# Performance work log

Hardware: AMD Instinct MI355X
Metric: run time of the kernel (lower is better)

Reference implementation:

```python
import jax, jax.numpy as jnp
import numpy as np

B, L, D = 2, 1024, 768
NH, HD = 12, 64
NL = 6
MLP = 3072
THETA = 10000.0


def _rope(pos, dim, theta):
    # pos: (L,) float -> (L, dim//2, 2, 2) rotation matrices (FLUX rope)
    omega = 1.0 / (theta ** (jnp.arange(0, dim, 2, dtype=jnp.float32) / dim))
    out = pos[:, None] * omega  # (L, dim//2)
    cos, sin = jnp.cos(out), jnp.sin(out)
    return jnp.stack([jnp.stack([cos, -sin], -1), jnp.stack([sin, cos], -1)], -2)


def _build_pe(seq_len, pe_dim):
    # 2D spatial ids: axis0 = x (fast), axis1 = y (slow); axes_dim = [pe_dim//2, pe_dim//2]
    h = w = int(seq_len ** 0.5)
    y_ids = jnp.repeat(jnp.arange(h, dtype=jnp.float32), w)
    x_ids = jnp.tile(jnp.arange(w, dtype=jnp.float32), h)
    half = pe_dim // 2
    pe = jnp.concatenate([_rope(x_ids, half, THETA), _rope(y_ids, half, THETA)], axis=-3)
    return pe[None, None]  # (1, 1, L, pe_dim//2, 2, 2)


def _apply_rope(x, pe):
    # x: (B, H, L, HD)
    xs = x.reshape(x.shape[:-1] + (-1, 1, 2))
    out = pe[..., 0] * xs[..., 0] + pe[..., 1] * xs[..., 1]
    return out.reshape(x.shape)


def _rmsnorm(x, scale):
    return x * jax.lax.rsqrt(jnp.mean(x * x, axis=-1, keepdims=True) + 1e-6) * scale


def _layernorm(x, g, b):
    m = jnp.mean(x, axis=-1, keepdims=True)
    v = jnp.var(x, axis=-1, keepdims=True)
    return (x - m) * jax.lax.rsqrt(v + 1e-5) * g + b


def _forward(spatial_features, density_weights, condition_embeddings,
             spatial_w, spatial_b, cond_w, cond_b,
             ln1_g, ln1_b, qkv_w, q_scale, k_scale, proj_w, proj_b,
             dscale, dbias, ln2_g, ln2_b, mlp_w1, mlp_b1, mlp_w2, mlp_b2,
             out_w, out_b):
    Bsz, Ls, Ds = spatial_features.shape
    x = spatial_features @ spatial_w + spatial_b
    x = x + (condition_embeddings @ cond_w + cond_b)[:, None, :]
    pe = _build_pe(Ls, HD)
    dflat = density_weights.reshape(Bsz, 1, Ls)  # H*W == L, no interpolation
    attn_scale = HD ** -0.5
    for i in range(NL):
        h = _layernorm(x, ln1_g[i], ln1_b[i])
        qkv = (h @ qkv_w[i]).reshape(Bsz, Ls, 3, NH, HD).transpose(2, 0, 3, 1, 4)
        q, k, v = qkv[0], qkv[1], qkv[2]
        q = _rmsnorm(q, q_scale[i])
        k = _rmsnorm(k, k_scale[i])
        q = _apply_rope(q, pe)
        k = _apply_rope(k, pe)
        scores = jnp.einsum('bhld,bhmd->bhlm', q, k) * attn_scale
        scores = scores + (dscale[i] * dflat[..., None] + dbias[i])  # (B,1,L,1) bcast
        attn = jax.nn.softmax(scores, axis=-1)
        o = jnp.einsum('bhlm,bhmd->bhld', attn, v)
        o = o.transpose(0, 2, 1, 3).reshape(Bsz, Ls, Ds)
        x = x + o @ proj_w[i] + proj_b[i]
        h2 = _layernorm(x, ln2_g[i], ln2_b[i])
        x = x + jax.nn.gelu(h2 @ mlp_w1[i] + mlp_b1[i], approximate=False) @ mlp_w2[i] + mlp_b2[i]
    return x @ out_w + out_b


def setup_inputs() -> dict:
    key = jax.random.key(0)
    ks = jax.random.split(key, 16)
    s = 0.02
    inp = {
        'spatial_features': jax.random.normal(ks[0], (B, L, D), jnp.float32),
        'density_weights': jax.random.uniform(ks[1], (B, 32, 32), jnp.float32),
        'condition_embeddings': jax.random.normal(ks[2], (B, 1536), jnp.float32),
        'spatial_w': jax.random.normal(ks[3], (D, D), jnp.float32) * s,
        'spatial_b': jnp.zeros((D,), jnp.float32),
        'cond_w': jax.random.normal(ks[4], (1536, D), jnp.float32) * s,
        'cond_b': jnp.zeros((D,), jnp.float32),
        'ln1_g': jnp.ones((NL, D), jnp.float32),
        'ln1_b': jnp.zeros((NL, D), jnp.float32),
        'qkv_w': jax.random.normal(ks[5], (NL, D, 3 * D), jnp.float32) * s,
        'q_scale': jnp.ones((NL, HD), jnp.float32),
        'k_scale': jnp.ones((NL, HD), jnp.float32),
        'proj_w': jax.random.normal(ks[6], (NL, D, D), jnp.float32) * s,
        'proj_b': jnp.zeros((NL, D), jnp.float32),
        'dscale': jnp.ones((NL,), jnp.float32),
        'dbias': jnp.zeros((NL,), jnp.float32),
        'ln2_g': jnp.ones((NL, D), jnp.float32),
        'ln2_b': jnp.zeros((NL, D), jnp.float32),
        'mlp_w1': jax.random.normal(ks[7], (NL, D, MLP), jnp.float32) * s,
        'mlp_b1': jnp.zeros((NL, MLP), jnp.float32),
        'mlp_w2': jax.random.normal(ks[8], (NL, MLP, D), jnp.float32) * s,
        'mlp_b2': jnp.zeros((NL, D), jnp.float32),
        'out_w': jax.random.normal(ks[9], (D, D), jnp.float32) * s,
        'out_b': jnp.zeros((D,), jnp.float32),
    }
    return inp


def reference(spatial_features, density_weights, condition_embeddings,
              spatial_w, spatial_b, cond_w, cond_b,
              ln1_g, ln1_b, qkv_w, q_scale, k_scale, proj_w, proj_b,
              dscale, dbias, ln2_g, ln2_b, mlp_w1, mlp_b1, mlp_w2, mlp_b2,
              out_w, out_b):
    return _forward(spatial_features, density_weights, condition_embeddings,
                    spatial_w, spatial_b, cond_w, cond_b,
                    ln1_g, ln1_b, qkv_w, q_scale, k_scale, proj_w, proj_b,
                    dscale, dbias, ln2_g, ln2_b, mlp_w1, mlp_b1, mlp_w2, mlp_b2,
                    out_w, out_b)
```

## Files before the change

kernel.cpp:

```cpp
#include <hip/hip_runtime.h>
#include <hip/hip_bf16.h>
#include <cstdint>
#include <cstddef>

typedef unsigned short u16;
using short8  = __attribute__((ext_vector_type(8))) short;
using floatx4 = __attribute__((ext_vector_type(4))) float;

typedef __attribute__((address_space(1))) void gvoid;
typedef __attribute__((address_space(3))) void svoid;

__device__ __forceinline__ u16 f2bf(float f) {
  __hip_bfloat16 h = __float2bfloat16(f);
  return __builtin_bit_cast(u16, h);
}

__device__ __forceinline__ floatx4 mfma16(short8 a, short8 b, floatx4 c) {
  return __builtin_amdgcn_mfma_f32_16x16x32_bf16(a, b, c, 0, 0, 0);
}

__device__ __forceinline__ void glds16(const u16* g, u16* l) {
  __builtin_amdgcn_global_load_lds((gvoid*)g, (svoid*)l, 16, 0, 0);
}

__global__ void pe_kernel(float* __restrict__ pet) {
  int t = blockIdx.x * 256 + threadIdx.x;
  if (t >= 32768) return;
  int l = t >> 5, j = t & 31;
  float pos   = (j < 16) ? (float)(l & 31) : (float)(l >> 5);
  float omega = powf(10000.f, -(float)(j & 15) / 16.f);
  float a = pos * omega;
  pet[2 * t]     = cosf(a);
  pet[2 * t + 1] = sinf(a);
}

__global__ __launch_bounds__(256) void twt_kernel(const float* __restrict__ in,
                                                  u16* __restrict__ out, int K, int N) {
  size_t lofs = (size_t)blockIdx.z * K * N;
  in  += lofs;
  out += lofs;
  __shared__ float tile[32][33];
  int bx = blockIdx.x;
  int by = blockIdx.y;
  int tx = threadIdx.x & 31, ty = threadIdx.x >> 5;
  #pragma unroll
  for (int p = 0; p < 4; p++) {
    int k = by * 32 + ty + p * 8;
    tile[ty + p * 8][tx] = in[(size_t)k * N + bx * 32 + tx];
  }
  __syncthreads();
  #pragma unroll
  for (int p = 0; p < 4; p++) {
    int n = bx * 32 + ty + p * 8;
    out[(size_t)n * K + by * 32 + tx] = f2bf(tile[tx][ty + p * 8]);
  }
}

__global__ void cvt_kernel(const float* __restrict__ in, u16* __restrict__ out, int n) {
  int i = blockIdx.x * 256 + threadIdx.x;
  if (i < n) out[i] = f2bf(in[i]);
}

__global__ __launch_bounds__(256) void condp_kernel(const float* __restrict__ ce,
                                                    const float* __restrict__ w,
                                                    float* __restrict__ partial) {
  int d = blockIdx.x * 256 + threadIdx.x;
  int c = blockIdx.y;
  #pragma unroll
  for (int b = 0; b < 2; b++) {
    float acc = 0.f;
    #pragma unroll 4
    for (int k = c * 96; k < c * 96 + 96; k++) acc += ce[b * 1536 + k] * w[(size_t)k * 768 + d];
    partial[(size_t)(c * 2 + b) * 768 + d] = acc;
  }
}

__global__ __launch_bounds__(256) void condr_kernel(const float* __restrict__ partial,
                                                    const float* __restrict__ bias,
                                                    float* __restrict__ out) {
  int t = blockIdx.x * 256 + threadIdx.x;
  int b = t / 768, d = t % 768;
  float acc = bias[d];
  #pragma unroll
  for (int c = 0; c < 16; c++) acc += partial[(size_t)(c * 2 + b) * 768 + d];
  out[b * 768 + d] = acc;
}

__global__ __launch_bounds__(256) void ln_kernel(const float* __restrict__ x,
                                                 const float* __restrict__ g,
                                                 const float* __restrict__ b,
                                                 u16* __restrict__ out) {
  int row = blockIdx.x;
  const float* xr = x + (size_t)row * 768;
  int t = threadIdx.x;
  float v0 = xr[t], v1 = xr[t + 256], v2 = xr[t + 512];
  float s = v0 + v1 + v2, s2 = v0 * v0 + v1 * v1 + v2 * v2;
  #pragma unroll
  for (int o = 32; o >= 1; o >>= 1) { s += __shfl_xor(s, o); s2 += __shfl_xor(s2, o); }
  __shared__ float red[8];
  int w = t >> 6, lane = t & 63;
  if (lane == 0) { red[w] = s; red[4 + w] = s2; }
  __syncthreads();
  s  = red[0] + red[1] + red[2] + red[3];
  s2 = red[4] + red[5] + red[6] + red[7];
  float mean = s * (1.f / 768.f);
  float var  = s2 * (1.f / 768.f) - mean * mean;
  float rstd = rsqrtf(var + 1e-5f);
  u16* orow = out + (size_t)row * 768;
  orow[t]       = f2bf((v0 - mean) * rstd * g[t] + b[t]);
  orow[t + 256] = f2bf((v1 - mean) * rstd * g[t + 256] + b[t + 256]);
  orow[t + 512] = f2bf((v2 - mean) * rstd * g[t + 512] + b[t + 512]);
}

__global__ __launch_bounds__(256) void rvt_kernel(const float* __restrict__ qkv,
                                                  const float* __restrict__ qs,
                                                  const float* __restrict__ ks,
                                                  const float* __restrict__ pet,
                                                  u16* __restrict__ qb, u16* __restrict__ kb,
                                                  u16* __restrict__ vt) {
  int lt = blockIdx.x, bh = blockIdx.y;
  int b = bh / 12, h = bh % 12;
  int t = threadIdx.x, lane = t & 63, w = t >> 6;

  #pragma unroll 2
  for (int r = 0; r < 16; r++) {
    int l = lt * 64 + w * 16 + r;
    const float* qp = qkv + ((size_t)(b * 1024 + l) * 3) * 768 + h * 64;
    const float* kp = qp + 768;
    float q = qp[lane], k = kp[lane];
    float sq = q * q, sk = k * k;
    #pragma unroll
    for (int o = 1; o < 64; o <<= 1) { sq += __shfl_xor(sq, o); sk += __shfl_xor(sk, o); }
    q *= rsqrtf(sq * (1.f / 64.f) + 1e-6f) * qs[lane];
    k *= rsqrtf(sk * (1.f / 64.f) + 1e-6f) * ks[lane];
    int j = lane >> 1;
    float c = pet[(l * 32 + j) * 2], s = pet[(l * 32 + j) * 2 + 1];
    float qo = __shfl_xor(q, 1), ko = __shfl_xor(k, 1);
    float qr = (lane & 1) ? (s * qo + c * q) : (c * q - s * qo);
    float kr = (lane & 1) ? (s * ko + c * k) : (c * k - s * ko);
    qb[((size_t)bh * 1024 + l) * 64 + lane] = f2bf(qr * 0.125f);
    kb[((size_t)bh * 1024 + l) * 64 + lane] = f2bf(kr);
  }

  __shared__ float tile[64][65];
  int c = t & 63, r0 = t >> 6;
  #pragma unroll
  for (int p = 0; p < 16; p++) {
    int lr = p * 4 + r0;
    tile[lr][c] = qkv[((size_t)(b * 1024 + lt * 64 + lr) * 3 + 2) * 768 + h * 64 + c];
  }
  __syncthreads();
  #pragma unroll
  for (int p = 0; p < 16; p++) {
    int d = p * 4 + r0;
    vt[((size_t)bh * 64 + d) * 1024 + lt * 64 + c] = f2bf(tile[c][d]);
  }
}

__global__ __launch_bounds__(256) void attn_split(const u16* __restrict__ qb,
                                                  const u16* __restrict__ kbuf,
                                                  const u16* __restrict__ vt,
                                                  float* __restrict__ po,
                                                  float* __restrict__ pl) {
  const int qt = blockIdx.x, bh = blockIdx.y, sp = blockIdx.z;
  const int lane = threadIdx.x & 63, w = threadIdx.x >> 6;
  const int quad = lane >> 4, l16 = lane & 15;
  __shared__ __align__(16) u16 Ks[128 * 64];
  __shared__ __align__(16) u16 Vs[64 * 128];
  __shared__ __align__(16) u16 Ps[4][16 * 136];
  const u16* Q  = qb   + (size_t)bh * 1024 * 64;
  const u16* Kp = kbuf + (size_t)bh * 1024 * 64;
  const u16* Vp = vt   + (size_t)bh * 64 * 1024;
  const int qrow0 = qt * 64 + w * 16;
  short8 aq0, aq1;
  {
    const u16* qp = Q + (size_t)(qrow0 + l16) * 64 + quad * 8;
    aq0 = *(const short8*)qp;
    aq1 = *(const short8*)(qp + 32);
  }
  floatx4 accO[4];
  #pragma unroll
  for (int i = 0; i < 4; i++) accO[i] = (floatx4){0.f, 0.f, 0.f, 0.f};
  float lsum[4] = {0.f, 0.f, 0.f, 0.f};

  const int krow_in = (lane >> 3);
  const int kchunk  = lane & 7;
  const int vrow_in = (lane >> 4);
  const int vchunk  = lane & 15;

  for (int nt = 0; nt < 4; ++nt) {
    const int kb0 = sp * 512 + nt * 128;
    __syncthreads();
    #pragma unroll
    for (int j = 0; j < 4; j++) {
      int r = w * 32 + j * 8 + krow_in;
      int g = kchunk ^ (r & 7);
      glds16(Kp + (size_t)(kb0 + r) * 64 + g * 8, Ks + (w * 32 + j * 8) * 64);
    }
    #pragma unroll
    for (int j = 0; j < 4; j++) {
      int r = w * 16 + j * 4 + vrow_in;
      int g = vchunk ^ (r & 15);
      glds16(Vp + (size_t)r * 1024 + kb0 + g * 8, Vs + (w * 16 + j * 4) * 128);
    }
    __syncthreads();

    floatx4 s[8];
    #pragma unroll
    for (int n = 0; n < 8; n++) {
      int row = n * 16 + l16;
      int c0 = quad ^ (l16 & 7);
      short8 b0 = *(const short8*)&Ks[row * 64 + c0 * 8];
      short8 b1 = *(const short8*)&Ks[row * 64 + (c0 ^ 4) * 8];
      floatx4 z = (floatx4){0.f, 0.f, 0.f, 0.f};
      z = mfma16(aq0, b0, z);
      s[n] = mfma16(aq1, b1, z);
    }
    #pragma unroll
    for (int n = 0; n < 8; n++) {
      #pragma unroll
      for (int r = 0; r < 4; r++) {
        float pv = __expf(s[n][r] - 8.f);
        lsum[r] += pv;
        Ps[w][(quad * 4 + r) * 136 + n * 16 + l16] = f2bf(pv);
      }
    }
    #pragma unroll
    for (int kt = 0; kt < 4; kt++) {
      short8 ap = *(const short8*)&Ps[w][l16 * 136 + kt * 32 + quad * 8];
      #pragma unroll
      for (int dt = 0; dt < 4; dt++) {
        int vrow = dt * 16 + l16;
        int c = (kt * 4 + quad) ^ l16;
        short8 bv = *(const short8*)&Vs[vrow * 128 + c * 8];
        accO[dt] = mfma16(ap, bv, accO[dt]);
      }
    }
  }
  #pragma unroll
  for (int r = 0; r < 4; r++) {
    #pragma unroll
    for (int o = 1; o < 16; o <<= 1) lsum[r] += __shfl_xor(lsum[r], o);
  }
  const size_t sb = (size_t)(sp * 24 + bh) * 1024;
  #pragma unroll
  for (int r = 0; r < 4; r++) {
    int lr = qrow0 + quad * 4 + r;
    if (l16 == 0) pl[sb + lr] = lsum[r];
    #pragma unroll
    for (int dt = 0; dt < 4; dt++)
      po[(sb + lr) * 64 + dt * 16 + l16] = accO[dt][r];
  }
}

__global__ __launch_bounds__(256) void attn_comb(const float* __restrict__ po,
                                                 const float* __restrict__ pl,
                                                 u16* __restrict__ obuf) {
  int w = threadIdx.x >> 6, lane = threadIdx.x & 63;
  int gr = blockIdx.x * 4 + w;
  int bh = gr >> 10, l = gr & 1023;
  float num = 0.f, den = 0.f;
  #pragma unroll
  for (int s = 0; s < 2; s++) {
    num += po[((size_t)(s * 24 + bh) * 1024 + l) * 64 + lane];
    den += pl[(size_t)(s * 24 + bh) * 1024 + l];
  }
  int b = bh / 12, h = bh % 12;
  obuf[((size_t)(b * 1024 + l)) * 768 + h * 64 + lane] = f2bf(num / den);
}

template <int EPI, int BM, int BN>
__global__ __launch_bounds__(256) void gemm_bt(const u16* __restrict__ A,
                                               const u16* __restrict__ Bt,
                                               const float* __restrict__ bias,
                                               const float* extra,
                                               float* Cf, u16* Cb, int M, int N, int K) {
  constexpr int ROWS = BM + BN;
  constexpr int RPW  = ROWS / 4;
  constexpr int NG   = RPW / 8;
  constexpr int MT   = BM / 32;
  constexpr int NTW  = BN / 32;
  __shared__ __align__(16) u16 S[2][ROWS * 64];
  const int t = threadIdx.x;
  const int lane = t & 63, w = t >> 6;
  const int quad = lane >> 4, l16 = lane & 15;
  const int m0 = blockIdx.y * BM, n0 = blockIdx.x * BN;
  const int wm = (w >> 1) * (BM / 2), wn = (w & 1) * (BN / 2);

  floatx4 acc[MT][NTW];
  #pragma unroll
  for (int i = 0; i < MT; i++)
    #pragma unroll
    for (int j = 0; j < NTW; j++) acc[i][j] = (floatx4){0.f, 0.f, 0.f, 0.f};

  const u16* gsrc[NG];
  int loff[NG];
  #pragma unroll
  for (int j = 0; j < NG; j++) {
    int r = w * RPW + j * 8 + (lane >> 3);
    int c = lane & 7;
    int g = c ^ (r & 7);
    const u16* base = (r < BM) ? (A + (size_t)(m0 + r) * K)
                               : (Bt + (size_t)(n0 + r - BM) * K);
    gsrc[j] = base + g * 8;
    loff[j] = (w * RPW + j * 8) * 64;
  }

  const int NIT = K >> 6;

  auto compute = [&](int buf) {
    const u16* Sb = &S[buf][0];
    #pragma unroll
    for (int kk = 0; kk < 2; kk++) {
      short8 af[MT], bfr[NTW];
      #pragma unroll
      for (int mt = 0; mt < MT; mt++) {
        int ra = wm + mt * 16 + l16;
        af[mt] = *(const short8*)&Sb[ra * 64 + ((((kk << 2) | quad)) ^ (ra & 7)) * 8];
      }
      #pragma unroll
      for (int nt = 0; nt < NTW; nt++) {
        int rb = BM + wn + nt * 16 + l16;
        bfr[nt] = *(const short8*)&Sb[rb * 64 + ((((kk << 2) | quad)) ^ (rb & 7)) * 8];
      }
      #pragma unroll
      for (int mt = 0; mt < MT; mt++)
        #pragma unroll
        for (int nt = 0; nt < NTW; nt++)
          acc[mt][nt] = mfma16(af[mt], bfr[nt], acc[mt][nt]);
    }
  };

  #pragma unroll
  for (int j = 0; j < NG; j++) glds16(gsrc[j], &S[0][loff[j]]);
  __syncthreads();

  int cur = 0;
  for (int it = 0; it < NIT; ++it) {
    if (it + 1 < NIT) {
      #pragma unroll
      for (int j = 0; j < NG; j++) glds16(gsrc[j] + (it + 1) * 64, &S[cur ^ 1][loff[j]]);
    }
    compute(cur);
    if (it + 1 < NIT) __syncthreads();
    cur ^= 1;
  }

  #pragma unroll
  for (int mt = 0; mt < MT; mt++) {
    #pragma unroll
    for (int nt = 0; nt < NTW; nt++) {
      int col = n0 + wn + nt * 16 + l16;
      float bcol = bias ? bias[col] : 0.f;
      #pragma unroll
      for (int r = 0; r < 4; r++) {
        int row = m0 + wm + mt * 16 + quad * 4 + r;
        float v = acc[mt][nt][r] + bcol;
        if (EPI == 1) v += extra[(row >> 10) * N + col];
        if (EPI == 2) v += extra[(size_t)row * N + col];
        if (EPI == 3) v = 0.5f * v * (1.f + erff(v * 0.70710678118654752f));
        if (Cf) Cf[(size_t)row * N + col] = v;
        if (Cb) Cb[(size_t)row * N + col] = f2bf(v);
      }
    }
  }
}

extern "C" void kernel_launch(void* const* d_in, const int* in_sizes, int n_in,
                              void* d_out, int out_size, void* d_ws, size_t ws_size,
                              hipStream_t stream) {
  const float* sf   = (const float*)d_in[0];
  const float* ce   = (const float*)d_in[2];
  const float* sw   = (const float*)d_in[3];
  const float* sb   = (const float*)d_in[4];
  const float* cw   = (const float*)d_in[5];
  const float* cb   = (const float*)d_in[6];
  const float* ln1g = (const float*)d_in[7];
  const float* ln1b = (const float*)d_in[8];
  const float* qkvw = (const float*)d_in[9];
  const float* qsc  = (const float*)d_in[10];
  const float* ksc  = (const float*)d_in[11];
  const float* pw   = (const float*)d_in[12];
  const float* pb   = (const float*)d_in[13];
  const float* ln2g = (const float*)d_in[16];
  const float* ln2b = (const float*)d_in[17];
  const float* w1   = (const float*)d_in[18];
  const float* b1   = (const float*)d_in[19];
  const float* w2   = (const float*)d_in[20];
  const float* b2   = (const float*)d_in[21];
  const float* ow   = (const float*)d_in[22];
  const float* ob   = (const float*)d_in[23];

  char* p = (char*)d_ws;
  auto alloc = [&](size_t bytes) { char* r = p; p += (bytes + 255) & ~(size_t)255; return r; };
  float* pet  = (float*)alloc((size_t)1024 * 32 * 2 * 4);
  u16* swT    = (u16*)alloc((size_t)768 * 768 * 2);
  u16* owT    = (u16*)alloc((size_t)768 * 768 * 2);
  u16* qkvT   = (u16*)alloc((size_t)6 * 2304 * 768 * 2);
  u16* pwT    = (u16*)alloc((size_t)6 * 768 * 768 * 2);
  u16* w1T    = (u16*)alloc((size_t)6 * 3072 * 768 * 2);
  u16* w2T    = (u16*)alloc((size_t)6 * 768 * 3072 * 2);
  u16* sfb    = (u16*)alloc((size_t)2048 * 768 * 2);
  float* cpar = (float*)alloc((size_t)32 * 768 * 4);
  float* cond = (float*)alloc((size_t)2 * 768 * 4);
  float* x    = (float*)alloc((size_t)2048 * 768 * 4);
  u16* xb     = (u16*)alloc((size_t)2048 * 768 * 2);
  u16* h      = (u16*)alloc((size_t)2048 * 768 * 2);
  float* qkv  = (float*)alloc((size_t)2048 * 2304 * 4);
  u16* qbuf   = (u16*)alloc((size_t)2048 * 768 * 2);
  u16* kbuf   = (u16*)alloc((size_t)2048 * 768 * 2);
  u16* vtb    = (u16*)alloc((size_t)2048 * 768 * 2);
  u16* obuf   = (u16*)alloc((size_t)2048 * 768 * 2);
  u16* gbuf   = (u16*)alloc((size_t)2048 * 3072 * 2);
  float* po   = (float*)alloc((size_t)2 * 24 * 1024 * 64 * 4);
  float* pl   = (float*)alloc((size_t)2 * 24 * 1024 * 4);

  pe_kernel<<<128, 256, 0, stream>>>(pet);
  twt_kernel<<<dim3(24, 24, 1), 256, 0, stream>>>(sw, swT, 768, 768);
  twt_kernel<<<dim3(24, 24, 1), 256, 0, stream>>>(ow, owT, 768, 768);
  twt_kernel<<<dim3(72, 24, 6), 256, 0, stream>>>(qkvw, qkvT, 768, 2304);
  twt_kernel<<<dim3(24, 24, 6), 256, 0, stream>>>(pw, pwT, 768, 768);
  twt_kernel<<<dim3(96, 24, 6), 256, 0, stream>>>(w1, w1T, 768, 3072);
  twt_kernel<<<dim3(24, 96, 6), 256, 0, stream>>>(w2, w2T, 3072, 768);
  cvt_kernel<<<(2048 * 768) / 256, 256, 0, stream>>>(sf, sfb, 2048 * 768);
  condp_kernel<<<dim3(3, 16), 256, 0, stream>>>(ce, cw, cpar);
  condr_kernel<<<6, 256, 0, stream>>>(cpar, cb, cond);

  gemm_bt<1, 64, 64><<<dim3(12, 32), 256, 0, stream>>>(sfb, swT, sb, cond, x, nullptr, 2048, 768, 768);

  for (int i = 0; i < 6; i++) {
    ln_kernel<<<2048, 256, 0, stream>>>(x, ln1g + i * 768, ln1b + i * 768, h);
    gemm_bt<0, 128, 128><<<dim3(18, 16), 256, 0, stream>>>(h, qkvT + (size_t)i * 2304 * 768,
                                                           nullptr, nullptr, qkv, nullptr, 2048, 2304, 768);
    rvt_kernel<<<dim3(16, 24), 256, 0, stream>>>(qkv, qsc + i * 64, ksc + i * 64, pet,
                                                 qbuf, kbuf, vtb);
    attn_split<<<dim3(16, 24, 2), 256, 0, stream>>>(qbuf, kbuf, vtb, po, pl);
    attn_comb<<<6144, 256, 0, stream>>>(po, pl, obuf);
    gemm_bt<2, 64, 64><<<dim3(12, 32), 256, 0, stream>>>(obuf, pwT + (size_t)i * 768 * 768,
                                                         pb + i * 768, x, x, xb, 2048, 768, 768);
    ln_kernel<<<2048, 256, 0, stream>>>(x, ln2g + i * 768, ln2b + i * 768, h);
    gemm_bt<3, 128, 128><<<dim3(24, 16), 256, 0, stream>>>(h, w1T + (size_t)i * 3072 * 768,
                                                           b1 + i * 3072, nullptr, nullptr, gbuf, 2048, 3072, 768);
    gemm_bt<2, 64, 64><<<dim3(12, 32), 256, 0, stream>>>(gbuf, w2T + (size_t)i * 768 * 3072,
                                                         b2 + i * 768, x, x, xb, 2048, 768, 3072);
  }
  gemm_bt<0, 64, 64><<<dim3(12, 32), 256, 0, stream>>>(xb, owT, ob, nullptr, (float*)d_out, nullptr,
                                                       2048, 768, 768);
}
```

Before: 1.071 ms.

## Shrink GEMM row tiles, split rope/V-transpose kernel, vectorize weight transpose

Every GEMM launch drops its M tile from 64/128 rows to 32 rows, so the grids become larger and the GPU's many compute units get more blocks to work on. The fused rope+V-transpose kernel is split in two: a per-row rope kernel with one wave per (token, head) and 6144 blocks, and a separate V transpose kernel. The one-time weight transpose now uses float4 loads and ushort4 stores. Smaller tiles mean less reuse per block and more redundant reads of B tiles, and the split adds one more kernel launch per layer.

Result: faster. 1.044 ms (-2.5%).

```diff
diff --git a/kernel.cpp b/kernel.cpp
--- a/kernel.cpp
+++ b/kernel.cpp
@@ -42,18 +42,17 @@
   __shared__ float tile[32][33];
   int bx = blockIdx.x;
   int by = blockIdx.y;
-  int tx = threadIdx.x & 31, ty = threadIdx.x >> 5;
-  #pragma unroll
-  for (int p = 0; p < 4; p++) {
-    int k = by * 32 + ty + p * 8;
-    tile[ty + p * 8][tx] = in[(size_t)k * N + bx * 32 + tx];
-  }
+  int t = threadIdx.x;
+  int lk = t >> 3, ln = (t & 7) * 4;
+  float4 v = *(const float4*)(in + (size_t)(by * 32 + lk) * N + bx * 32 + ln);
+  tile[lk][ln + 0] = v.x; tile[lk][ln + 1] = v.y;
+  tile[lk][ln + 2] = v.z; tile[lk][ln + 3] = v.w;
   __syncthreads();
-  #pragma unroll
-  for (int p = 0; p < 4; p++) {
-    int n = bx * 32 + ty + p * 8;
-    out[(size_t)n * K + by * 32 + tx] = f2bf(tile[tx][ty + p * 8]);
-  }
+  int n = t >> 3, k0 = (t & 7) * 4;
+  ushort4 o;
+  o.x = f2bf(tile[k0 + 0][n]); o.y = f2bf(tile[k0 + 1][n]);
+  o.z = f2bf(tile[k0 + 2][n]); o.w = f2bf(tile[k0 + 3][n]);
+  *(ushort4*)(out + (size_t)(bx * 32 + n) * K + by * 32 + k0) = o;
 }
 
 __global__ void cvt_kernel(const float* __restrict__ in, u16* __restrict__ out, int n) {
@@ -112,38 +111,39 @@
   orow[t + 512] = f2bf((v2 - mean) * rstd * g[t + 512] + b[t + 512]);
 }
 
-__global__ __launch_bounds__(256) void rvt_kernel(const float* __restrict__ qkv,
-                                                  const float* __restrict__ qs,
-                                                  const float* __restrict__ ks,
-                                                  const float* __restrict__ pet,
-                                                  u16* __restrict__ qb, u16* __restrict__ kb,
-                                                  u16* __restrict__ vt) {
+__global__ __launch_bounds__(256) void ropeq_kernel(const float* __restrict__ qkv,
+                                                    const float* __restrict__ qs,
+                                                    const float* __restrict__ ks,
+                                                    const float* __restrict__ pet,
+                                                    u16* __restrict__ qb, u16* __restrict__ kb) {
+  int gid = blockIdx.x * 4 + (threadIdx.x >> 6);
+  int lane = threadIdx.x & 63;
+  int h = gid % 12, bl = gid / 12;
+  int l = bl & 1023, b = bl >> 10;
+  const float* qp = qkv + ((size_t)(b * 1024 + l) * 3 + 0) * 768 + h * 64;
+  const float* kp = qp + 768;
+  float q = qp[lane], k = kp[lane];
+  float sq = q * q, sk = k * k;
+  #pragma unroll
+  for (int o = 1; o < 64; o <<= 1) { sq += __shfl_xor(sq, o); sk += __shfl_xor(sk, o); }
+  q *= rsqrtf(sq * (1.f / 64.f) + 1e-6f) * qs[lane];
+  k *= rsqrtf(sk * (1.f / 64.f) + 1e-6f) * ks[lane];
+  int j = lane >> 1;
+  float c = pet[(l * 32 + j) * 2], s = pet[(l * 32 + j) * 2 + 1];
+  float qo = __shfl_xor(q, 1), ko = __shfl_xor(k, 1);
+  float qr = (lane & 1) ? (s * qo + c * q) : (c * q - s * qo);
+  float kr = (lane & 1) ? (s * ko + c * k) : (c * k - s * ko);
+  int bh = b * 12 + h;
+  qb[((size_t)bh * 1024 + l) * 64 + lane] = f2bf(qr * 0.125f);
+  kb[((size_t)bh * 1024 + l) * 64 + lane] = f2bf(kr);
+}
+
+__global__ __launch_bounds__(256) void vtrans_kernel(const float* __restrict__ qkv,
+                                                     u16* __restrict__ vt) {
   int lt = blockIdx.x, bh = blockIdx.y;
   int b = bh / 12, h = bh % 12;
-  int t = threadIdx.x, lane = t & 63, w = t >> 6;
-
-  #pragma unroll 2
-  for (int r = 0; r < 16; r++) {
-    int l = lt * 64 + w * 16 + r;
-    const float* qp = qkv + ((size_t)(b * 1024 + l) * 3) * 768 + h * 64;
-    const float* kp = qp + 768;
-    float q = qp[lane], k = kp[lane];
-    float sq = q * q, sk = k * k;
-    #pragma unroll
-    for (int o = 1; o < 64; o <<= 1) { sq += __shfl_xor(sq, o); sk += __shfl_xor(sk, o); }
-    q *= rsqrtf(sq * (1.f / 64.f) + 1e-6f) * qs[lane];
-    k *= rsqrtf(sk * (1.f / 64.f) + 1e-6f) * ks[lane];
-    int j = lane >> 1;
-    float c = pet[(l * 32 + j) * 2], s = pet[(l * 32 + j) * 2 + 1];
-    float qo = __shfl_xor(q, 1), ko = __shfl_xor(k, 1);
-    float qr = (lane & 1) ? (s * qo + c * q) : (c * q - s * qo);
-    float kr = (lane & 1) ? (s * ko + c * k) : (c * k - s * ko);
-    qb[((size_t)bh * 1024 + l) * 64 + lane] = f2bf(qr * 0.125f);
-    kb[((size_t)bh * 1024 + l) * 64 + lane] = f2bf(kr);
-  }
-
   __shared__ float tile[64][65];
-  int c = t & 63, r0 = t >> 6;
+  int t = threadIdx.x, c = t & 63, r0 = t >> 6;
   #pragma unroll
   for (int p = 0; p < 16; p++) {
     int lr = p * 4 + r0;
@@ -426,24 +426,24 @@
   condp_kernel<<<dim3(3, 16), 256, 0, stream>>>(ce, cw, cpar);
   condr_kernel<<<6, 256, 0, stream>>>(cpar, cb, cond);
 
-  gemm_bt<1, 64, 64><<<dim3(12, 32), 256, 0, stream>>>(sfb, swT, sb, cond, x, nullptr, 2048, 768, 768);
+  gemm_bt<1, 32, 64><<<dim3(12, 64), 256, 0, stream>>>(sfb, swT, sb, cond, x, nullptr, 2048, 768, 768);
 
   for (int i = 0; i < 6; i++) {
     ln_kernel<<<2048, 256, 0, stream>>>(x, ln1g + i * 768, ln1b + i * 768, h);
-    gemm_bt<0, 128, 128><<<dim3(18, 16), 256, 0, stream>>>(h, qkvT + (size_t)i * 2304 * 768,
-                                                           nullptr, nullptr, qkv, nullptr, 2048, 2304, 768);
-    rvt_kernel<<<dim3(16, 24), 256, 0, stream>>>(qkv, qsc + i * 64, ksc + i * 64, pet,
-                                                 qbuf, kbuf, vtb);
+    gemm_bt<0, 32, 128><<<dim3(18, 64), 256, 0, stream>>>(h, qkvT + (size_t)i * 2304 * 768,
+                                                          nullptr, nullptr, qkv, nullptr, 2048, 2304, 768);
+    ropeq_kernel<<<6144, 256, 0, stream>>>(qkv, qsc + i * 64, ksc + i * 64, pet, qbuf, kbuf);
+    vtrans_kernel<<<dim3(16, 24), 256, 0, stream>>>(qkv, vtb);
     attn_split<<<dim3(16, 24, 2), 256, 0, stream>>>(qbuf, kbuf, vtb, po, pl);
     attn_comb<<<6144, 256, 0, stream>>>(po, pl, obuf);
-    gemm_bt<2, 64, 64><<<dim3(12, 32), 256, 0, stream>>>(obuf, pwT + (size_t)i * 768 * 768,
+    gemm_bt<2, 32, 64><<<dim3(12, 64), 256, 0, stream>>>(obuf, pwT + (size_t)i * 768 * 768,
                                                          pb + i * 768, x, x, xb, 2048, 768, 768);
     ln_kernel<<<2048, 256, 0, stream>>>(x, ln2g + i * 768, ln2b + i * 768, h);
-    gemm_bt<3, 128, 128><<<dim3(24, 16), 256, 0, stream>>>(h, w1T + (size_t)i * 3072 * 768,
-                                                           b1 + i * 3072, nullptr, nullptr, gbuf, 2048, 3072, 768);
-    gemm_bt<2, 64, 64><<<dim3(12, 32), 256, 0, stream>>>(gbuf, w2T + (size_t)i * 768 * 3072,
+    gemm_bt<3, 32, 128><<<dim3(24, 64), 256, 0, stream>>>(h, w1T + (size_t)i * 3072 * 768,
+                                                          b1 + i * 3072, nullptr, nullptr, gbuf, 2048, 3072, 768);
+    gemm_bt<2, 32, 64><<<dim3(12, 64), 256, 0, stream>>>(gbuf, w2T + (size_t)i * 768 * 3072,
                                                          b2 + i * 768, x, x, xb, 2048, 768, 3072);
   }
-  gemm_bt<0, 64, 64><<<dim3(12, 32), 256, 0, stream>>>(xb, owT, ob, nullptr, (float*)d_out, nullptr,
+  gemm_bt<0, 32, 64><<<dim3(12, 64), 256, 0, stream>>>(xb, owT, ob, nullptr, (float*)d_out, nullptr,
                                                        2048, 768, 768);
 }
```
